# Kernel optimization log

Hardware: AMD Instinct MI355X
Metric: run time of the kernel (lower is better)

The kernel has to match this reference:

```python
import jax, jax.numpy as jnp
import numpy as np

NUM_CLASSES = 81
THRESHOLD = 0.5
NEGPOS_RATIO = 3
OBJ_SCORE = 0.01
VAR0, VAR1 = 0.1, 0.2


def point_form(boxes):
    # center form (cx,cy,w,h) -> corner form (x1,y1,x2,y2)
    return jnp.concatenate([boxes[:, :2] - boxes[:, 2:] / 2,
                            boxes[:, :2] + boxes[:, 2:] / 2], axis=1)


def jaccard(a, b):
    # a: [A,4] corners, b: [B,4] corners -> IoU [A,B]
    lt = jnp.maximum(a[:, None, :2], b[None, :, :2])
    rb = jnp.minimum(a[:, None, 2:], b[None, :, 2:])
    wh = jnp.clip(rb - lt, 0.0)
    inter = wh[..., 0] * wh[..., 1]
    area_a = ((a[:, 2] - a[:, 0]) * (a[:, 3] - a[:, 1]))[:, None]
    area_b = ((b[:, 2] - b[:, 0]) * (b[:, 3] - b[:, 1]))[None, :]
    return inter / (area_a + area_b - inter)


def encode(matched, priors):
    # matched: [P,4] corner-form GT, priors: [P,4] center-form
    g_cxcy = ((matched[:, :2] + matched[:, 2:]) / 2 - priors[:, :2]) / (VAR0 * priors[:, 2:])
    g_wh = jnp.log((matched[:, 2:] - matched[:, :2]) / priors[:, 2:]) / VAR1
    return jnp.concatenate([g_cxcy, g_wh], axis=1)


def match_one(truths, labels, priors):
    # truths: [O,4] corners, labels: [O] int, priors: [P,4] center-form
    overlaps = jaccard(truths, point_form(priors))      # [O,P]
    best_prior_idx = jnp.argmax(overlaps, axis=1)       # [O]
    best_truth_overlap = jnp.max(overlaps, axis=0)      # [P]
    best_truth_idx = jnp.argmax(overlaps, axis=0)       # [P]
    # ensure every gt matches its best prior
    best_truth_overlap = best_truth_overlap.at[best_prior_idx].set(2.0)
    best_truth_idx = best_truth_idx.at[best_prior_idx].set(jnp.arange(truths.shape[0]))
    matches = truths[best_truth_idx]                    # [P,4]
    conf = jnp.where(best_truth_overlap < THRESHOLD, 0, labels[best_truth_idx].astype(jnp.int32))
    return encode(matches, priors), conf


def smooth_l1(x):
    ax = jnp.abs(x)
    return jnp.where(ax < 1.0, 0.5 * ax * ax, ax - 0.5)


def ce_per_row(logits, tgt):
    # sum-reduction cross-entropy components: logsumexp - logit[target]
    lse = jax.nn.logsumexp(logits, axis=-1)
    picked = jnp.take_along_axis(logits, tgt[..., None].astype(jnp.int32), axis=-1)[..., 0]
    return lse - picked


def setup_inputs() -> dict:
    key = jax.random.key(0)
    ks = jax.random.split(key, 8)
    B, P, O, C = 32, 24564, 16, NUM_CLASSES
    loc_data = jax.random.normal(ks[0], (B, P, 4), jnp.float32)
    conf_data = jax.random.normal(ks[1], (B, P, C), jnp.float32)
    obj_data = jax.random.normal(ks[2], (B, P, 2), jnp.float32)
    # priors in center form
    pc = jax.random.uniform(ks[3], (P, 2), jnp.float32, 0.0, 1.0)
    pwh = jax.random.uniform(ks[4], (P, 2), jnp.float32, 0.05, 0.5)
    priors = jnp.concatenate([pc, pwh], axis=1)
    # gt boxes in corner form, valid (x1<x2, y1<y2)
    tc = jax.random.uniform(ks[5], (B, O, 2), jnp.float32, 0.2, 0.8)
    twh = jax.random.uniform(ks[6], (B, O, 2), jnp.float32, 0.05, 0.3)
    truths = jnp.concatenate([jnp.clip(tc - twh / 2, 0.0, 1.0),
                              jnp.clip(tc + twh / 2, 0.0, 1.0)], axis=-1)
    labels = jax.random.randint(ks[7], (B, O), 1, C).astype(jnp.int64)
    return {"loc_data": loc_data, "conf_data": conf_data, "obj_data": obj_data,
            "priors": priors, "truths": truths, "labels": labels}


def reference(loc_data, conf_data, obj_data, priors, truths, labels):
    num, num_priors = loc_data.shape[:2]
    loc_t, conf_t = jax.vmap(match_one, in_axes=(0, 0, None))(truths, labels, priors)
    loc_t = jax.lax.stop_gradient(loc_t)      # Variable(requires_grad=False)
    conf_t = jax.lax.stop_gradient(conf_t)
    obj_t = (conf_t > 0).astype(jnp.int32)

    obj_conf = jax.lax.stop_gradient(obj_data[:, :, 1])   # .detach()
    pos = conf_t > 0
    # faithful to original (buggy) filter: (pos + neg_positive) > 2 is never true
    neg_positive = (pos.astype(jnp.int32) + (obj_conf < OBJ_SCORE).astype(jnp.int32)) > 2
    pos = pos & ~neg_positive
    pos = jnp.where(pos.sum() == 0, conf_t > 0, pos)

    # localization loss (smooth L1, sum over positives)
    l1 = smooth_l1(loc_data - loc_t).sum(-1)               # [B,P]
    loss_l = jnp.sum(jnp.where(pos, l1, 0.0))

    # objectness loss with hard negative mining
    ce_obj = ce_per_row(obj_data, obj_t)                   # [B,P]
    pos_obj = obj_t > 0
    mining_obj = jnp.where(pos_obj, 0.0, jax.lax.stop_gradient(ce_obj))
    rank_obj = jnp.argsort(jnp.argsort(-mining_obj, axis=1), axis=1)
    num_obj_pos = pos_obj.sum(1, keepdims=True)
    num_obj_neg = jnp.minimum(NEGPOS_RATIO * num_obj_pos, num_priors - 1)
    neg_obj = rank_obj < num_obj_neg
    loss_obj = jnp.sum(jnp.where(pos_obj | neg_obj, ce_obj, 0.0))

    # class confidence loss with hard negative mining
    ce_c = ce_per_row(conf_data, conf_t)                   # [B,P]
    mining_c = jnp.where(pos, 0.0, jax.lax.stop_gradient(ce_c))
    rank_c = jnp.argsort(jnp.argsort(-mining_c, axis=1), axis=1)
    num_pos = pos.sum(1, keepdims=True)
    num_neg = jnp.minimum(NEGPOS_RATIO * num_pos, num_priors - 1)
    neg = rank_c < num_neg
    loss_c = jnp.sum(jnp.where(pos | neg, ce_c, 0.0))

    N = jnp.maximum(num_pos.sum(), 1).astype(loc_data.dtype)
    N1 = jnp.maximum(num_obj_neg.sum(), 1).astype(loc_data.dtype)
    return (loss_l / N, loss_c / N, 0.4 * loss_obj / N1)
```

## Files before the change

kernel.cpp:

```cpp
#include <hip/hip_runtime.h>
#include <hip/hip_bf16.h>
#include <math.h>

#define BB 32
#define PP 24564
#define OO 16
#define CC 81
#define BP (BB * PP)
#define CHUNK 1024

typedef unsigned long long ull;

__device__ __forceinline__ float sl1(float x) {
    float ax = fabsf(x);
    return ax < 1.0f ? 0.5f * ax * ax : ax - 0.5f;
}

__global__ __launch_bounds__(256) void k_match_a(
        const float* __restrict__ priors, const float* __restrict__ truths,
        float* __restrict__ bto, int* __restrict__ bti,
        ull* __restrict__ best_prior ) {
    const int b = blockIdx.y;
    const int p0 = blockIdx.x * CHUNK;
    const int tid = threadIdx.x;
    __shared__ float tr[OO][4];
    __shared__ float tarea[OO];
    __shared__ ull red[4][OO];
    if (tid < OO * 4) ((float*)tr)[tid] = truths[b * OO * 4 + tid];
    __syncthreads();
    if (tid < OO) tarea[tid] = (tr[tid][2] - tr[tid][0]) * (tr[tid][3] - tr[tid][1]);
    __syncthreads();

    float bpv[OO];
    int bpi[OO];
#pragma unroll
    for (int o = 0; o < OO; o++) { bpv[o] = -1.0f; bpi[o] = -1; }

    const int pend = (p0 + CHUNK < PP) ? p0 + CHUNK : PP;
    for (int p = p0 + tid; p < pend; p += 256) {
        const float4 pr = ((const float4*)priors)[p];
        const float x1 = pr.x - pr.z * 0.5f, y1 = pr.y - pr.w * 0.5f;
        const float x2 = pr.x + pr.z * 0.5f, y2 = pr.y + pr.w * 0.5f;
        const float parea = (x2 - x1) * (y2 - y1);
        float best = -1.0f;
        int bidx = 0;
#pragma unroll
        for (int o = 0; o < OO; o++) {
            const float lx = fmaxf(tr[o][0], x1), ly = fmaxf(tr[o][1], y1);
            const float rx = fminf(tr[o][2], x2), ry = fminf(tr[o][3], y2);
            const float iw = fmaxf(rx - lx, 0.0f), ih = fmaxf(ry - ly, 0.0f);
            const float inter = iw * ih;
            const float iou = inter / (tarea[o] + parea - inter);
            if (iou > best) { best = iou; bidx = o; }
            if (iou > bpv[o]) { bpv[o] = iou; bpi[o] = p; }
        }
        bto[(size_t)b * PP + p] = best;
        bti[(size_t)b * PP + p] = bidx;
    }

    const int wave = tid >> 6;
    const int lane = tid & 63;
#pragma unroll
    for (int o = 0; o < OO; o++) {
        ull key = (bpi[o] >= 0)
            ? (((ull)__float_as_uint(bpv[o]) << 32) |
               (ull)(0xFFFFFFFFu - (unsigned)bpi[o]))
            : 0ull;
#pragma unroll
        for (int d = 32; d; d >>= 1) {
            const ull other = __shfl_xor(key, d);
            key = (other > key) ? other : key;
        }
        if (lane == 0) red[wave][o] = key;
    }
    __syncthreads();
    if (tid < OO) {
        const ull k0 = red[0][tid], k1 = red[1][tid];
        const ull k2 = red[2][tid], k3 = red[3][tid];
        ull m = k0 > k1 ? k0 : k1;
        const ull m2 = k2 > k3 ? k2 : k3;
        m = m > m2 ? m : m2;
        if (m != 0ull) atomicMax(&best_prior[b * OO + tid], m);
    }
}

__global__ void k_match_b(const ull* __restrict__ best_prior,
                          float* __restrict__ bto, int* __restrict__ bti) {
    const int b = threadIdx.x;
    if (b >= BB) return;
    for (int o = 0; o < OO; o++) {
        const unsigned p = 0xFFFFFFFFu - (unsigned)(best_prior[b * OO + o] & 0xFFFFFFFFull);
        bto[(size_t)b * PP + p] = 2.0f;
        bti[(size_t)b * PP + p] = o;
    }
}

__global__ __launch_bounds__(256) void k_ce(
        const float* __restrict__ conf, const float* __restrict__ obj,
        const float* __restrict__ loc, const float* __restrict__ priors,
        const float* __restrict__ truths, const int* __restrict__ labels,
        const float* __restrict__ bto, const int* __restrict__ bti,
        float* __restrict__ mining_obj, float* __restrict__ mining_c,
        int* __restrict__ num_posS ,
        float* __restrict__ accS  ) {
    const int tid = threadIdx.x;
    const int row0 = blockIdx.x * 64;
    __shared__ float sconf[64 * CC];
    __shared__ float slse[64];

    const float4* src = (const float4*)(conf + (size_t)row0 * CC);
    float4* dst = (float4*)sconf;
    for (int i = tid; i < (64 * CC) / 4; i += 256) dst[i] = src[i];
    __syncthreads();

    const int r = tid >> 2;
    const int part = tid & 3;
    const float* rowp = sconf + r * CC;
    const int c0 = part * 20;
    const int c1 = (part == 3) ? CC : c0 + 20;
    float m = -INFINITY;
    for (int c = c0; c < c1; c++) m = fmaxf(m, rowp[c]);
    m = fmaxf(m, __shfl_xor(m, 1));
    m = fmaxf(m, __shfl_xor(m, 2));
    float s = 0.0f;
    for (int c = c0; c < c1; c++) s += __expf(rowp[c] - m);
    s += __shfl_xor(s, 1);
    s += __shfl_xor(s, 2);
    if (part == 0) slse[r] = m + __logf(s);
    __syncthreads();

    if (tid < 64) {
        const int row = row0 + tid;
        const int b = row / PP;
        const int p = row - b * PP;
        const float ov = bto[row];
        const int ti = bti[row];
        const int lbl = labels[b * OO + ti];
        const int tgt = (ov < 0.5f) ? 0 : lbl;
        const float ce_c = slse[tid] - sconf[tid * CC + tgt];

        const float2 o2 = ((const float2*)obj)[row];
        const float mo = fmaxf(o2.x, o2.y);
        const float lse_o = mo + __logf(__expf(o2.x - mo) + __expf(o2.y - mo));
        const bool pos = tgt > 0;
        const float ce_o = lse_o - (pos ? o2.y : o2.x);

        mining_c[row]   = pos ? 0.0f : ce_c;
        mining_obj[row] = pos ? 0.0f : ce_o;

        float my_l = 0.0f, my_co = 0.0f, my_cc = 0.0f;
        if (pos) {
            my_co = ce_o;
            my_cc = ce_c;
            const float4 pr = ((const float4*)priors)[p];
            const float4 t  = ((const float4*)truths)[b * OO + ti];
            const float gcx = ((t.x + t.z) * 0.5f - pr.x) / (0.1f * pr.z);
            const float gcy = ((t.y + t.w) * 0.5f - pr.y) / (0.1f * pr.w);
            const float gw = logf((t.z - t.x) / pr.z) / 0.2f;
            const float gh = logf((t.w - t.y) / pr.w) / 0.2f;
            const float4 ld = ((const float4*)loc)[row];
            my_l = sl1(ld.x - gcx) + sl1(ld.y - gcy) +
                   sl1(ld.z - gw) + sl1(ld.w - gh);
        }

        const int b0 = row0 / PP;
        const ull mpos = __ballot(pos);
        const ull mb1  = __ballot(b != b0);
#pragma unroll
        for (int d = 32; d; d >>= 1) {
            my_l  += __shfl_down(my_l,  d);
            my_co += __shfl_down(my_co, d);
            my_cc += __shfl_down(my_cc, d);
        }
        if (tid == 0 && mpos) {
            const int cnt0 = __popcll(mpos & ~mb1);
            const int cnt1 = __popcll(mpos &  mb1);
            int* nps = num_posS + (blockIdx.x & 7) * BB;
            if (cnt0) atomicAdd(&nps[b0], cnt0);
            if (cnt1) atomicAdd(&nps[b0 + 1], cnt1);
            float* slot = accS + (size_t)(blockIdx.x & 63) * 32;
            atomicAdd(slot + 0, my_l);
            atomicAdd(slot + 1, my_co);
            atomicAdd(slot + 2, my_cc);
        }
    }
}

__global__ __launch_bounds__(1024) void k_select(
        const float* __restrict__ mining ,
        const int* __restrict__ num_posS ,
        float* __restrict__ acc,
        int* __restrict__ n1_acc) {
    const int arr = blockIdx.x >> 5;
    const int b = blockIdx.x & 31;
    const int tid = threadIdx.x;
    const float* x = mining + ((size_t)arr * BB + b) * PP;
    int np = 0;
#pragma unroll
    for (int s = 0; s < 8; s++) np += num_posS[s * BB + b];
    long long k64 = 3LL * np;
    const int k = (int)(k64 < (long long)(PP - 1) ? k64 : (long long)(PP - 1));
    if (tid == 0 && arr == 0) atomicAdd(n1_acc, k);
    if (k <= 0) return;

    __shared__ unsigned hist[256];
    __shared__ unsigned s_prefix;
    __shared__ int s_krem;
    __shared__ float wsum[16];
    __shared__ unsigned wcnt[16];
    if (tid == 0) { s_prefix = 0u; s_krem = k; }

    for (int shift = 24; shift >= 0; shift -= 8) {
        __syncthreads();
        if (tid < 256) hist[tid] = 0u;
        const unsigned prefix = s_prefix;
        const unsigned pmask = (shift == 24) ? 0u : (0xFFFFFFFFu << (shift + 8));
        __syncthreads();
        for (int i = tid; i < PP; i += 1024) {
            const unsigned u = __float_as_uint(x[i]);
            if ((u & pmask) == prefix)
                atomicAdd(&hist[(u >> shift) & 255u], 1u);
        }
        __syncthreads();
        if (tid == 0) {
            const int krem = s_krem;
            unsigned cum = 0;
            int sel = 0;
            for (int byte = 255; byte >= 0; byte--) {
                const unsigned h = hist[byte];
                if (cum + h >= (unsigned)krem) { sel = byte; break; }
                cum += h;
            }
            s_krem = krem - (int)cum;
            s_prefix = prefix | ((unsigned)sel << shift);
        }
    }
    __syncthreads();

    const unsigned t = s_prefix;
    float lsum = 0.0f;
    unsigned lcnt = 0;
    for (int i = tid; i < PP; i += 1024) {
        const float v = x[i];
        if (__float_as_uint(v) > t) { lsum += v; lcnt++; }
    }
#pragma unroll
    for (int d = 32; d; d >>= 1) {
        lsum += __shfl_down(lsum, d);
        lcnt += __shfl_down(lcnt, d);
    }
    const int wave = tid >> 6;
    if ((tid & 63) == 0) { wsum[wave] = lsum; wcnt[wave] = lcnt; }
    __syncthreads();
    if (tid == 0) {
        float ts = 0.0f;
        unsigned tc = 0;
#pragma unroll
        for (int w = 0; w < 16; w++) { ts += wsum[w]; tc += wcnt[w]; }
        const float tsum = ts + (float)(k - (int)tc) * __uint_as_float(t);
        atomicAdd(&acc[3 + arr], tsum);
    }
}

__global__ void k_final(const float* __restrict__ acc,
                        const float* __restrict__ accS ,
                        const int* __restrict__ num_posS ,
                        const int* __restrict__ n1_acc,
                        float* __restrict__ out) {
    const int t = threadIdx.x;
    float sl = accS[t * 32 + 0];
    float so = accS[t * 32 + 1];
    float sc = accS[t * 32 + 2];
    int np = 0;
#pragma unroll
    for (int i = 0; i < 4; i++) np += num_posS[t + i * 64];
#pragma unroll
    for (int d = 32; d; d >>= 1) {
        sl += __shfl_down(sl, d);
        so += __shfl_down(so, d);
        sc += __shfl_down(sc, d);
        np += __shfl_down(np, d);
    }
    if (t == 0) {
        const float fN = (float)(np > 1 ? np : 1);
        const int n1 = *n1_acc;
        const float fN1 = (float)(n1 > 1 ? n1 : 1);
        out[0] = sl / fN;
        out[1] = (sc + acc[4]) / fN;
        out[2] = 0.4f * (so + acc[3]) / fN1;
    }
}

extern "C" void kernel_launch(void* const* d_in, const int* in_sizes, int n_in,
                              void* d_out, int out_size, void* d_ws, size_t ws_size,
                              hipStream_t stream) {
    const float* loc_data  = (const float*)d_in[0];
    const float* conf_data = (const float*)d_in[1];
    const float* obj_data  = (const float*)d_in[2];
    const float* priors    = (const float*)d_in[3];
    const float* truths    = (const float*)d_in[4];
    const int*   labels    = (const int*)d_in[5];
    float* out = (float*)d_out;

    float* ws_f = (float*)d_ws;
    float* bto = ws_f;
    int*   bti = (int*)(ws_f + BP);
    float* mining = ws_f + 2 * (size_t)BP;
    ull*   best_prior = (ull*)(ws_f + 4 * (size_t)BP);
    int*   num_posS = (int*)(ws_f + 4 * (size_t)BP + 1024);
    float* acc = ws_f + 4 * (size_t)BP + 1280;
    int*   n1_acc = (int*)(ws_f + 4 * (size_t)BP + 1288);
    float* accS = ws_f + 4 * (size_t)BP + 2048;

    hipMemsetAsync((void*)best_prior, 0, 16384, stream);

    dim3 mg((PP + CHUNK - 1) / CHUNK, BB);
    k_match_a<<<mg, 256, 0, stream>>>(priors, truths, bto, bti, best_prior);
    k_match_b<<<1, 32, 0, stream>>>(best_prior, bto, bti);

    k_ce<<<BP / 64, 256, 0, stream>>>(conf_data, obj_data, loc_data, priors,
                                      truths, labels, bto, bti,
                                      mining , mining + BP ,
                                      num_posS, accS);

    k_select<<<64, 1024, 0, stream>>>(mining, num_posS, acc, n1_acc);

    k_final<<<1, 64, 0, stream>>>(acc, accS, num_posS, n1_acc, out);
}
```

Baseline: 459.9 us.

## Recompute best-truth match inside CE kernel and privatize select histograms per wave

k_match_a now only computes each ground truth's best prior. The per-prior best-truth IoU and index are recomputed in k_ce from truths, labels and best-prior indices staged in shared memory. This removes the bto/bti global arrays and the k_match_b launch, trading write and read traffic for repeated IoU arithmetic. Separately, k_select's radix-select histogram is split into per-wave shared histograms that are summed afterward, to cut shared-atomic contention at the cost of more shared memory and a reduction step.

Measured after the change: 464.7 us. Within noise of the previous version (+1.1%).

```diff
diff --git a/kernel.cpp b/kernel.cpp
--- a/kernel.cpp
+++ b/kernel.cpp
@@ -18,7 +18,6 @@
 
 __global__ __launch_bounds__(256) void k_match_a(
         const float* __restrict__ priors, const float* __restrict__ truths,
-        float* __restrict__ bto, int* __restrict__ bti,
         ull* __restrict__ best_prior ) {
     const int b = blockIdx.y;
     const int p0 = blockIdx.x * CHUNK;
@@ -42,8 +41,6 @@
         const float x1 = pr.x - pr.z * 0.5f, y1 = pr.y - pr.w * 0.5f;
         const float x2 = pr.x + pr.z * 0.5f, y2 = pr.y + pr.w * 0.5f;
         const float parea = (x2 - x1) * (y2 - y1);
-        float best = -1.0f;
-        int bidx = 0;
 #pragma unroll
         for (int o = 0; o < OO; o++) {
             const float lx = fmaxf(tr[o][0], x1), ly = fmaxf(tr[o][1], y1);
@@ -51,11 +48,8 @@
             const float iw = fmaxf(rx - lx, 0.0f), ih = fmaxf(ry - ly, 0.0f);
             const float inter = iw * ih;
             const float iou = inter / (tarea[o] + parea - inter);
-            if (iou > best) { best = iou; bidx = o; }
             if (iou > bpv[o]) { bpv[o] = iou; bpi[o] = p; }
         }
-        bto[(size_t)b * PP + p] = best;
-        bti[(size_t)b * PP + p] = bidx;
     }
 
     const int wave = tid >> 6;
@@ -84,29 +78,34 @@
     }
 }
 
-__global__ void k_match_b(const ull* __restrict__ best_prior,
-                          float* __restrict__ bto, int* __restrict__ bti) {
-    const int b = threadIdx.x;
-    if (b >= BB) return;
-    for (int o = 0; o < OO; o++) {
-        const unsigned p = 0xFFFFFFFFu - (unsigned)(best_prior[b * OO + o] & 0xFFFFFFFFull);
-        bto[(size_t)b * PP + p] = 2.0f;
-        bti[(size_t)b * PP + p] = o;
-    }
-}
-
 __global__ __launch_bounds__(256) void k_ce(
         const float* __restrict__ conf, const float* __restrict__ obj,
         const float* __restrict__ loc, const float* __restrict__ priors,
         const float* __restrict__ truths, const int* __restrict__ labels,
-        const float* __restrict__ bto, const int* __restrict__ bti,
+        const ull* __restrict__ best_prior,
         float* __restrict__ mining_obj, float* __restrict__ mining_c,
         int* __restrict__ num_posS ,
         float* __restrict__ accS  ) {
     const int tid = threadIdx.x;
     const int row0 = blockIdx.x * 64;
+    const int b0 = row0 / PP;
     __shared__ float sconf[64 * CC];
     __shared__ float slse[64];
+    __shared__ float4 s_tr[2][OO];
+    __shared__ float  s_ta[2][OO];
+    __shared__ int    s_lb[2][OO];
+    __shared__ unsigned s_fp[2][OO];
+
+    const int nb = ((row0 - b0 * PP) + 64 > PP) ? 2 : 1;
+    if (tid < nb * OO) {
+        const int bb = tid >> 4, o = tid & 15;
+        const float4 t = ((const float4*)truths)[(b0 + bb) * OO + o];
+        s_tr[bb][o] = t;
+        s_ta[bb][o] = (t.z - t.x) * (t.w - t.y);
+        s_lb[bb][o] = labels[(b0 + bb) * OO + o];
+        s_fp[bb][o] = 0xFFFFFFFFu -
+            (unsigned)(best_prior[(b0 + bb) * OO + o] & 0xFFFFFFFFull);
+    }
 
     const float4* src = (const float4*)(conf + (size_t)row0 * CC);
     float4* dst = (float4*)sconf;
@@ -132,10 +131,32 @@
     if (tid < 64) {
         const int row = row0 + tid;
         const int b = row / PP;
+        const int lb_i = b - b0;
         const int p = row - b * PP;
-        const float ov = bto[row];
-        const int ti = bti[row];
-        const int lbl = labels[b * OO + ti];
+
+        const float4 pr = ((const float4*)priors)[p];
+        const float x1 = pr.x - pr.z * 0.5f, y1 = pr.y - pr.w * 0.5f;
+        const float x2 = pr.x + pr.z * 0.5f, y2 = pr.y + pr.w * 0.5f;
+        const float parea = (x2 - x1) * (y2 - y1);
+        float best = -1.0f;
+        int ti = 0;
+#pragma unroll
+        for (int o = 0; o < OO; o++) {
+            const float4 t = s_tr[lb_i][o];
+            const float lx = fmaxf(t.x, x1), ly = fmaxf(t.y, y1);
+            const float rx = fminf(t.z, x2), ry = fminf(t.w, y2);
+            const float iw = fmaxf(rx - lx, 0.0f), ih = fmaxf(ry - ly, 0.0f);
+            const float inter = iw * ih;
+            const float iou = inter / (s_ta[lb_i][o] + parea - inter);
+            if (iou > best) { best = iou; ti = o; }
+        }
+        float ov = best;
+#pragma unroll
+        for (int o = 0; o < OO; o++) {
+            if (s_fp[lb_i][o] == (unsigned)p) { ti = o; ov = 2.0f; }
+        }
+
+        const int lbl = s_lb[lb_i][ti];
         const int tgt = (ov < 0.5f) ? 0 : lbl;
         const float ce_c = slse[tid] - sconf[tid * CC + tgt];
 
@@ -152,8 +173,7 @@
         if (pos) {
             my_co = ce_o;
             my_cc = ce_c;
-            const float4 pr = ((const float4*)priors)[p];
-            const float4 t  = ((const float4*)truths)[b * OO + ti];
+            const float4 t = s_tr[lb_i][ti];
             const float gcx = ((t.x + t.z) * 0.5f - pr.x) / (0.1f * pr.z);
             const float gcy = ((t.y + t.w) * 0.5f - pr.y) / (0.1f * pr.w);
             const float gw = logf((t.z - t.x) / pr.z) / 0.2f;
@@ -163,7 +183,6 @@
                    sl1(ld.z - gw) + sl1(ld.w - gh);
         }
 
-        const int b0 = row0 / PP;
         const ull mpos = __ballot(pos);
         const ull mb1  = __ballot(b != b0);
 #pragma unroll
@@ -194,6 +213,7 @@
     const int arr = blockIdx.x >> 5;
     const int b = blockIdx.x & 31;
     const int tid = threadIdx.x;
+    const int wv = tid >> 6;
     const float* x = mining + ((size_t)arr * BB + b) * PP;
     int np = 0;
 #pragma unroll
@@ -203,6 +223,7 @@
     if (tid == 0 && arr == 0) atomicAdd(n1_acc, k);
     if (k <= 0) return;
 
+    __shared__ unsigned histw[16][256];
     __shared__ unsigned hist[256];
     __shared__ unsigned s_prefix;
     __shared__ int s_krem;
@@ -212,14 +233,21 @@
 
     for (int shift = 24; shift >= 0; shift -= 8) {
         __syncthreads();
-        if (tid < 256) hist[tid] = 0u;
+        for (int i = tid; i < 16 * 256; i += 1024) ((unsigned*)histw)[i] = 0u;
         const unsigned prefix = s_prefix;
         const unsigned pmask = (shift == 24) ? 0u : (0xFFFFFFFFu << (shift + 8));
         __syncthreads();
         for (int i = tid; i < PP; i += 1024) {
             const unsigned u = __float_as_uint(x[i]);
             if ((u & pmask) == prefix)
-                atomicAdd(&hist[(u >> shift) & 255u], 1u);
+                atomicAdd(&histw[wv][(u >> shift) & 255u], 1u);
+        }
+        __syncthreads();
+        if (tid < 256) {
+            unsigned s = 0;
+#pragma unroll
+            for (int w = 0; w < 16; w++) s += histw[w][tid];
+            hist[tid] = s;
         }
         __syncthreads();
         if (tid == 0) {
@@ -249,8 +277,7 @@
         lsum += __shfl_down(lsum, d);
         lcnt += __shfl_down(lcnt, d);
     }
-    const int wave = tid >> 6;
-    if ((tid & 63) == 0) { wsum[wave] = lsum; wcnt[wave] = lcnt; }
+    if ((tid & 63) == 0) { wsum[wv] = lsum; wcnt[wv] = lcnt; }
     __syncthreads();
     if (tid == 0) {
         float ts = 0.0f;
@@ -303,23 +330,20 @@
     float* out = (float*)d_out;
 
     float* ws_f = (float*)d_ws;
-    float* bto = ws_f;
-    int*   bti = (int*)(ws_f + BP);
-    float* mining = ws_f + 2 * (size_t)BP;
-    ull*   best_prior = (ull*)(ws_f + 4 * (size_t)BP);
-    int*   num_posS = (int*)(ws_f + 4 * (size_t)BP + 1024);
-    float* acc = ws_f + 4 * (size_t)BP + 1280;
-    int*   n1_acc = (int*)(ws_f + 4 * (size_t)BP + 1288);
-    float* accS = ws_f + 4 * (size_t)BP + 2048;
+    float* mining = ws_f;
+    ull*   best_prior = (ull*)(ws_f + 2 * (size_t)BP);
+    int*   num_posS = (int*)(ws_f + 2 * (size_t)BP + 1024);
+    float* acc = ws_f + 2 * (size_t)BP + 1280;
+    int*   n1_acc = (int*)(ws_f + 2 * (size_t)BP + 1288);
+    float* accS = ws_f + 2 * (size_t)BP + 2048;
 
     hipMemsetAsync((void*)best_prior, 0, 16384, stream);
 
     dim3 mg((PP + CHUNK - 1) / CHUNK, BB);
-    k_match_a<<<mg, 256, 0, stream>>>(priors, truths, bto, bti, best_prior);
-    k_match_b<<<1, 32, 0, stream>>>(best_prior, bto, bti);
+    k_match_a<<<mg, 256, 0, stream>>>(priors, truths, best_prior);
 
     k_ce<<<BP / 64, 256, 0, stream>>>(conf_data, obj_data, loc_data, priors,
-                                      truths, labels, bto, bti,
+                                      truths, labels, best_prior,
                                       mining , mining + BP ,
                                       num_posS, accS);
 
```
